# Performance work log

Measured on AMD Instinct MI355X. Metric: run time of the kernel, lower is better.

The kernel has to match this reference:

```python
import jax, jax.numpy as jnp
import numpy as np

# FlowNetC correlation config (kernel_size=1 -> pointwise patch; pad == max_displacement)
PAD = 20
MAX_DISP = 20
STRIDE2 = 2


def setup_inputs() -> dict:
    key = jax.random.key(0)
    k1, k2 = jax.random.split(key)
    B, C, H, W = 4, 256, 96, 96
    input1 = jax.random.normal(k1, (B, C, H, W), dtype=jnp.float32)
    input2 = jax.random.normal(k2, (B, C, H, W), dtype=jnp.float32)
    return {"input1": input1, "input2": input2}


def _correlation(x1, x2):
    # x1, x2: [B, C, H, W]. Output: [B, D*D, H, W] with D = 2*MAX_DISP//STRIDE2 + 1.
    B, C, H, W = x1.shape
    x2p = jnp.pad(x2, ((0, 0), (0, 0), (PAD, PAD), (PAD, PAD)))
    D = 2 * MAX_DISP // STRIDE2 + 1  # 21
    # start index into padded map = PAD + (disp) where disp = off - MAX_DISP;
    # since PAD == MAX_DISP, start index == off.
    offs = jnp.arange(D, dtype=jnp.int32) * STRIDE2
    dyv, dxv = jnp.meshgrid(offs, offs, indexing="ij")
    pairs = jnp.stack([dyv.ravel(), dxv.ravel()], axis=1)  # [D*D, 2]
    inv_c = jnp.float32(1.0 / C)  # CUDA kernel divides by kernel^2 * C (kernel=1)

    def body(_, p):
        dy, dx = p[0], p[1]
        sl = jax.lax.dynamic_slice(x2p, (0, 0, dy, dx), (B, C, H, W))
        return None, jnp.einsum("bchw,bchw->bhw", x1, sl) * inv_c

    _, corr = jax.lax.scan(body, None, pairs)  # [D*D, B, H, W]
    return corr.transpose(1, 0, 2, 3)  # [B, D*D, H, W]


def reference(input1, input2):
    return _correlation(input1, input2)
```

## Files before the change

kernel.cpp:

```cpp
#include <hip/hip_runtime.h>
#include <hip/hip_bf16.h>


typedef __bf16 bf16x8 __attribute__((ext_vector_type(8)));
typedef float f32x4 __attribute__((ext_vector_type(4)));

#define B_ 4
#define C_ 256
#define H_ 96
#define W_ 96
#define NOFF 21
#define ROWS 96
#define IMG_ELEMS (ROWS * C_)
#define X1T_ELEMS (B_ * H_ * IMG_ELEMS)

__device__ __forceinline__ unsigned short f32_to_bf16_rne(float f) {
    union { float f; unsigned u; } v; v.f = f;
    unsigned u = v.u;
    return (unsigned short)((u + 0x7fffu + ((u >> 16) & 1u)) >> 16);
}

__device__ __forceinline__ void gl2lds16(const void* g, void* l) {
    __builtin_amdgcn_global_load_lds(
        (const __attribute__((address_space(1))) void*)g,
        (__attribute__((address_space(3))) void*)l, 16, 0, 0);
}

__global__ __launch_bounds__(256) void prep_kernel(const float* __restrict__ x1,
                                                   const float* __restrict__ x2,
                                                   unsigned short* __restrict__ ws) {
    __shared__ float tile[96 * 65];
    int bid = blockIdx.x;
    int cblk  = bid & 3;
    int which = (bid >> 2) & 1;
    int bh    = bid >> 3;
    int h = bh % H_;
    int b = bh / H_;
    int c0 = cblk << 6;

    const float* src = (which ? x2 : x1) + ((size_t)(b * C_ + c0) * H_ + h) * W_;
    unsigned short* dst = ws + (size_t)which * X1T_ELEMS + (size_t)(b * H_ + h) * IMG_ELEMS;

    for (int idx = threadIdx.x; idx < 64 * 96; idx += 256) {
        int c = idx / 96, w = idx - c * 96;
        tile[w * 65 + c] = src[c * (H_ * W_) + w];
    }
    __syncthreads();

    for (int idx = threadIdx.x; idx < 96 * 8; idx += 256) {
        int row = idx >> 3, tp = idx & 7;
        int par = row / 48, i = row - par * 48;
        int w = 2 * i + par;
        int s = tp ^ (row & 7);
        const float* fsrc = &tile[w * 65 + (s << 3)];
        unsigned pk[4];
#pragma unroll
        for (int e = 0; e < 4; ++e) {
            unsigned lo = f32_to_bf16_rne(fsrc[2 * e]);
            unsigned hi = f32_to_bf16_rne(fsrc[2 * e + 1]);
            pk[e] = lo | (hi << 16);
        }
        int ccp = (((c0 >> 3) ^ (row & 24)) + tp);
        *(uint4*)((char*)(dst + (size_t)row * C_) + (ccp << 4)) =
            make_uint4(pk[0], pk[1], pk[2], pk[3]);
    }
}

__global__ __launch_bounds__(384, 2) void corr_kernel(const unsigned short* __restrict__ ws,
                                                      float* __restrict__ out) {
    __shared__ unsigned short Bs[3][IMG_ELEMS];
    __shared__ float sl[2][NOFF][97];
    static_assert(sizeof(Bs) + sizeof(sl) <= 163840, "LDS budget");

    int bid = blockIdx.x;
    int xcd = bid & 7, sidx = bid >> 3;
    int b  = xcd >> 1;
    int p  = ((xcd & 1) ? 24 : 0) + (sidx >> 2);
    int og = sidx & 3;
    int g = p >> 1, par_h = p & 1;
    int hA = 4 * g + par_h, hB = hA + 2;
    int olo = (og * NOFF) >> 2;
    int ohi = ((og + 1) * NOFF) >> 2;

    int tid = threadIdx.x;
    int wv = tid >> 6, lane = tid & 63;
    int par = wv & 1, mt = wv >> 1;
    int i0 = mt << 4;
    int n = lane & 15, quad = lane >> 4;

    int jcnt = 5 + (tid < 96 ? 1 : 0);
    int slotj[6], offj[6]; bool mj[6];
#pragma unroll
    for (int j = 0; j < 6; ++j) {
        int idx = tid + j * 384;
        int ox = idx / W_, w = idx - ox * W_;
        slotj[j] = ox * 97 + w;
        offj[j]  = ox * (H_ * W_) + w;
        int w2 = w + 2 * ox - 20;
        mj[j] = (w2 >= 0) & (w2 < W_);
    }

    int rowA = par * 48 + i0 + n;
    int keyA = rowA & 31;
    const unsigned short* AgA = ws + (size_t)(b * H_ + hA) * IMG_ELEMS + (size_t)rowA * C_;
    const unsigned short* AgB = ws + (size_t)(b * H_ + hB) * IMG_ELEMS + (size_t)rowA * C_;
    bf16x8 afA[8], afB[8];
#pragma unroll
    for (int ks = 0; ks < 8; ++ks) {
        int o = (((ks << 2) | quad) ^ keyA) << 3;
        afA[ks] = *(const bf16x8*)(AgA + o);
        afB[ks] = *(const bf16x8*)(AgB + o);
    }

    const unsigned short* Bimg = ws + (size_t)X1T_ELEMS + (size_t)(b * H_) * IMG_ELEMS;

    int rowB0 = par * 48 + n;
    int rowB1 = rowB0 + 16;
    int rowB2 = rowB0 + 32;
    int keyB0 = rowB0 & 31, keyB1 = rowB1 & 31, keyB2 = rowB2 & 31;

    int aLo = (hA <= 20) ? ((21 - hA) >> 1) : 0; if (aLo < olo) aLo = olo;
    int aHi = ((115 - hA) >> 1) + 1;             if (aHi > ohi) aHi = ohi;
    if (aHi < aLo) aHi = aLo;
    int bLo = (hB <= 20) ? ((21 - hB) >> 1) : 0; if (bLo < olo) bLo = olo;
    int bHi = ((115 - hB) >> 1) + 1;             if (bHi > ohi) bHi = ohi;
    if (bHi < bLo) bHi = bLo;

    int tlo, thi;
    bool ea = (aLo >= aHi), eb = (bLo >= bHi);
    if (ea && eb)      { tlo = 0; thi = 0; }
    else if (ea)       { tlo = bLo + 1; thi = bHi + 1; }
    else if (eb)       { tlo = aLo; thi = aHi; }
    else {
        tlo = (aLo < bLo + 1) ? aLo : bLo + 1;
        thi = (aHi > bHi + 1) ? aHi : bHi + 1;
    }
    int nv = thi - tlo;

    int wvoff  = wv * 8192;
    int gmaoff = wvoff + lane * 16;

    if (nv > 0) {
        const char* Bg = (const char*)(Bimg + (size_t)(hA + 2 * tlo - 20) * IMG_ELEMS);
#pragma unroll
        for (int c = 0; c < 8; ++c)
            gl2lds16(Bg + gmaoff + c * 1024, (char*)Bs[0] + wvoff + c * 1024);
    }
    if (nv > 1) {
        const char* Bg = (const char*)(Bimg + (size_t)(hA + 2 * (tlo + 1) - 20) * IMG_ELEMS);
#pragma unroll
        for (int c = 0; c < 8; ++c)
            gl2lds16(Bg + gmaoff + c * 1024, (char*)Bs[1] + wvoff + c * 1024);
    }

    for (int oy = olo; oy < ohi; ++oy) {
        if (oy < aLo || oy >= aHi) {
            int outb = ((b * 441 + oy * NOFF) * H_ + hA) * W_;
#pragma unroll
            for (int j = 0; j < 6; ++j) if (j < jcnt) out[outb + offj[j]] = 0.0f;
        }
        if (oy < bLo || oy >= bHi) {
            int outb = ((b * 441 + oy * NOFF) * H_ + hB) * W_;
#pragma unroll
            for (int j = 0; j < 6; ++j) if (j < jcnt) out[outb + offj[j]] = 0.0f;
        }
    }

    const float* slA = &sl[0][0][0];
    const float* slB = &sl[1][0][0];

    for (int k = 0; k < nv; ++k) {
        int t = tlo + k;
        int cur = k % 3;

        if (k + 2 < nv) {
            int nb = (k + 2) % 3;
            const char* Bg = (const char*)(Bimg + (size_t)(hA + 2 * (t + 2) - 20) * IMG_ELEMS);
#pragma unroll
            for (int c = 0; c < 8; ++c)
                gl2lds16(Bg + gmaoff + c * 1024, (char*)Bs[nb] + wvoff + c * 1024);
        }

        if (k == 0) {
            if (nv > 2)       asm volatile("s_waitcnt vmcnt(16)\ns_barrier" ::: "memory");
            else if (nv == 2) asm volatile("s_waitcnt vmcnt(8)\ns_barrier" ::: "memory");
            else              asm volatile("s_waitcnt vmcnt(0)\ns_barrier" ::: "memory");
        } else if (k + 2 < nv) {
            asm volatile("s_waitcnt vmcnt(21)\ns_barrier" ::: "memory");
        } else if (k + 1 < nv) {
            asm volatile("s_waitcnt vmcnt(13)\ns_barrier" ::: "memory");
        } else {
            asm volatile("s_waitcnt vmcnt(5)\ns_barrier" ::: "memory");
        }

        const char* Bsb = (const char*)Bs[cur];
        f32x4 aA0 = {0.f,0.f,0.f,0.f}, aA1 = {0.f,0.f,0.f,0.f}, aA2 = {0.f,0.f,0.f,0.f};
        f32x4 aB0 = {0.f,0.f,0.f,0.f}, aB1 = {0.f,0.f,0.f,0.f}, aB2 = {0.f,0.f,0.f,0.f};

        if (mt == 0) {
            bf16x8 f0[8], f1[8];
#pragma unroll
            for (int ks = 0; ks < 8; ++ks) {
                int ci = (ks << 2) | quad;
                f0[ks] = *(const bf16x8*)(Bsb + rowB0 * 512 + ((ci ^ keyB0) << 4));
                f1[ks] = *(const bf16x8*)(Bsb + rowB1 * 512 + ((ci ^ keyB1) << 4));
            }
#pragma unroll
            for (int ks = 0; ks < 8; ++ks) {
                aA0 = __builtin_amdgcn_mfma_f32_16x16x32_bf16(afA[ks], f0[ks], aA0, 0, 0, 0);
                aA1 = __builtin_amdgcn_mfma_f32_16x16x32_bf16(afA[ks], f1[ks], aA1, 0, 0, 0);
                aB0 = __builtin_amdgcn_mfma_f32_16x16x32_bf16(afB[ks], f0[ks], aB0, 0, 0, 0);
                aB1 = __builtin_amdgcn_mfma_f32_16x16x32_bf16(afB[ks], f1[ks], aB1, 0, 0, 0);
            }
        } else if (mt == 1) {
            bf16x8 f0[8], f1[8], f2[8];
#pragma unroll
            for (int ks = 0; ks < 8; ++ks) {
                int ci = (ks << 2) | quad;
                f0[ks] = *(const bf16x8*)(Bsb + rowB0 * 512 + ((ci ^ keyB0) << 4));
                f1[ks] = *(const bf16x8*)(Bsb + rowB1 * 512 + ((ci ^ keyB1) << 4));
                f2[ks] = *(const bf16x8*)(Bsb + rowB2 * 512 + ((ci ^ keyB2) << 4));
            }
#pragma unroll
            for (int ks = 0; ks < 8; ++ks) {
                aA0 = __builtin_amdgcn_mfma_f32_16x16x32_bf16(afA[ks], f0[ks], aA0, 0, 0, 0);
                aA1 = __builtin_amdgcn_mfma_f32_16x16x32_bf16(afA[ks], f1[ks], aA1, 0, 0, 0);
                aA2 = __builtin_amdgcn_mfma_f32_16x16x32_bf16(afA[ks], f2[ks], aA2, 0, 0, 0);
                aB0 = __builtin_amdgcn_mfma_f32_16x16x32_bf16(afB[ks], f0[ks], aB0, 0, 0, 0);
                aB1 = __builtin_amdgcn_mfma_f32_16x16x32_bf16(afB[ks], f1[ks], aB1, 0, 0, 0);
                aB2 = __builtin_amdgcn_mfma_f32_16x16x32_bf16(afB[ks], f2[ks], aB2, 0, 0, 0);
            }
        } else {
            bf16x8 f1[8], f2[8];
#pragma unroll
            for (int ks = 0; ks < 8; ++ks) {
                int ci = (ks << 2) | quad;
                f1[ks] = *(const bf16x8*)(Bsb + rowB1 * 512 + ((ci ^ keyB1) << 4));
                f2[ks] = *(const bf16x8*)(Bsb + rowB2 * 512 + ((ci ^ keyB2) << 4));
            }
#pragma unroll
            for (int ks = 0; ks < 8; ++ks) {
                aA1 = __builtin_amdgcn_mfma_f32_16x16x32_bf16(afA[ks], f1[ks], aA1, 0, 0, 0);
                aA2 = __builtin_amdgcn_mfma_f32_16x16x32_bf16(afA[ks], f2[ks], aA2, 0, 0, 0);
                aB1 = __builtin_amdgcn_mfma_f32_16x16x32_bf16(afB[ks], f1[ks], aB1, 0, 0, 0);
                aB2 = __builtin_amdgcn_mfma_f32_16x16x32_bf16(afB[ks], f2[ks], aB2, 0, 0, 0);
            }
        }

#pragma unroll
        for (int r = 0; r < 4; ++r) {
            int m = (quad << 2) + r;
            int w = 2 * (i0 + m) + par;
            int oxb = n - i0 - m - 6;
            if (mt != 2) { int ox = 16 + oxb; if (ox >= 0 && ox < NOFF) { sl[0][ox][w] = aA0[r]; sl[1][ox][w] = aB0[r]; } }
            {             int ox = 32 + oxb; if (ox >= 0 && ox < NOFF) { sl[0][ox][w] = aA1[r]; sl[1][ox][w] = aB1[r]; } }
            if (mt != 0) { int ox = 48 + oxb; if (ox >= 0 && ox < NOFF) { sl[0][ox][w] = aA2[r]; sl[1][ox][w] = aB2[r]; } }
        }

        asm volatile("s_waitcnt lgkmcnt(0)\ns_barrier" ::: "memory");

        bool okA = (t >= aLo) & (t < aHi);
        bool okB = (t - 1 >= bLo) & (t - 1 < bHi);
        int outbA = ((b * 441 + t * NOFF) * H_ + hA) * W_;
        int outbB = ((b * 441 + (t - 1) * NOFF) * H_ + hB) * W_;

        float vA[6], vB[6];
#pragma unroll
        for (int j = 0; j < 6; ++j) if (j < jcnt) {
            vA[j] = mj[j] ? slA[slotj[j]] * (1.0f / 256.0f) : 0.0f;
            vB[j] = mj[j] ? slB[slotj[j]] * (1.0f / 256.0f) : 0.0f;
        }
        if (okA) {
#pragma unroll
            for (int j = 0; j < 6; ++j) if (j < jcnt) out[outbA + offj[j]] = vA[j];
        }
        if (okB) {
#pragma unroll
            for (int j = 0; j < 6; ++j) if (j < jcnt) out[outbB + offj[j]] = vB[j];
        }
    }
}

__global__ __launch_bounds__(256) void corr_fallback(const float* __restrict__ x1,
                                                     const float* __restrict__ x2,
                                                     float* __restrict__ out) {
    int bid = blockIdx.x;
    int oy = bid % NOFF, h = (bid / NOFF) % H_, b = bid / (NOFF * H_);
    int dy = 2 * oy - 20, h2 = h + dy;
    int outbase = ((b * 441 + oy * NOFF) * H_ + h) * W_;
    for (int idx = threadIdx.x; idx < NOFF * W_; idx += 256) {
        int ox = idx / W_, w = idx % W_;
        float acc = 0.f;
        int w2 = w + 2 * ox - 20;
        if (h2 >= 0 && h2 < H_ && w2 >= 0 && w2 < W_) {
            const float* p1 = x1 + (size_t)b * C_ * H_ * W_ + h * W_ + w;
            const float* p2 = x2 + (size_t)b * C_ * H_ * W_ + h2 * W_ + w2;
            for (int c = 0; c < C_; ++c) acc += p1[c * (H_ * W_)] * p2[c * (H_ * W_)];
        }
        out[outbase + ox * (H_ * W_) + w] = acc * (1.0f / 256.0f);
    }
}

extern "C" void kernel_launch(void* const* d_in, const int* in_sizes, int n_in,
                              void* d_out, int out_size, void* d_ws, size_t ws_size,
                              hipStream_t stream) {
    const float* x1 = (const float*)d_in[0];
    const float* x2 = (const float*)d_in[1];
    float* out = (float*)d_out;

    size_t need = (size_t)2 * X1T_ELEMS * sizeof(unsigned short);
    if (ws_size >= need) {
        unsigned short* ws = (unsigned short*)d_ws;
        prep_kernel<<<B_ * H_ * 2 * 4, 256, 0, stream>>>(x1, x2, ws);
        corr_kernel<<<768, 384, 0, stream>>>(ws, out);
    } else {
        corr_fallback<<<B_ * H_ * NOFF, 256, 0, stream>>>(x1, x2, out);
    }
}
```

Baseline: 164.6 us.

## Single-buffer LDS tile to fit more blocks per CU, prefetch after barrier

```diff
diff --git a/kernel.cpp b/kernel.cpp
--- a/kernel.cpp
+++ b/kernel.cpp
@@ -66,11 +66,11 @@
     }
 }
 
-__global__ __launch_bounds__(384, 2) void corr_kernel(const unsigned short* __restrict__ ws,
+__global__ __launch_bounds__(384, 3) void corr_kernel(const unsigned short* __restrict__ ws,
                                                       float* __restrict__ out) {
-    __shared__ unsigned short Bs[3][IMG_ELEMS];
+    __shared__ unsigned short Bs[IMG_ELEMS];
     __shared__ float sl[2][NOFF][97];
-    static_assert(sizeof(Bs) + sizeof(sl) <= 163840, "LDS budget");
+    static_assert(sizeof(Bs) + sizeof(sl) <= 81920, "need 2 blocks/CU");
 
     int bid = blockIdx.x;
     int xcd = bid & 7, sidx = bid >> 3;
@@ -111,6 +111,8 @@
         afA[ks] = *(const bf16x8*)(AgA + o);
         afB[ks] = *(const bf16x8*)(AgB + o);
     }
+    asm volatile("" ::: "memory");
+    __builtin_amdgcn_s_waitcnt(0);
 
     const unsigned short* Bimg = ws + (size_t)X1T_ELEMS + (size_t)(b * H_) * IMG_ELEMS;
 
@@ -140,18 +142,15 @@
     int wvoff  = wv * 8192;
     int gmaoff = wvoff + lane * 16;
 
-    if (nv > 0) {
-        const char* Bg = (const char*)(Bimg + (size_t)(hA + 2 * tlo - 20) * IMG_ELEMS);
-#pragma unroll
-        for (int c = 0; c < 8; ++c)
-            gl2lds16(Bg + gmaoff + c * 1024, (char*)Bs[0] + wvoff + c * 1024);
-    }
-    if (nv > 1) {
-        const char* Bg = (const char*)(Bimg + (size_t)(hA + 2 * (tlo + 1) - 20) * IMG_ELEMS);
-#pragma unroll
-        for (int c = 0; c < 8; ++c)
-            gl2lds16(Bg + gmaoff + c * 1024, (char*)Bs[1] + wvoff + c * 1024);
-    }
+#define STAGE(tt) do {                                                                \
+    const char* Bg_ = (const char*)(Bimg + (size_t)(hA + 2 * (tt) - 20) * IMG_ELEMS); \
+    _Pragma("unroll")                                                                 \
+    for (int c = 0; c < 8; ++c)                                                       \
+        gl2lds16(Bg_ + gmaoff + c * 1024, (char*)Bs + wvoff + c * 1024);              \
+} while (0)
+
+    if (nv > 0) STAGE(tlo);
+    asm volatile("" ::: "memory");
 
     for (int oy = olo; oy < ohi; ++oy) {
         if (oy < aLo || oy >= aHi) {
@@ -171,32 +170,15 @@
 
     for (int k = 0; k < nv; ++k) {
         int t = tlo + k;
-        int cur = k % 3;
-
-        if (k + 2 < nv) {
-            int nb = (k + 2) % 3;
-            const char* Bg = (const char*)(Bimg + (size_t)(hA + 2 * (t + 2) - 20) * IMG_ELEMS);
-#pragma unroll
-            for (int c = 0; c < 8; ++c)
-                gl2lds16(Bg + gmaoff + c * 1024, (char*)Bs[nb] + wvoff + c * 1024);
-        }
-
-        if (k == 0) {
-            if (nv > 2)       asm volatile("s_waitcnt vmcnt(16)\ns_barrier" ::: "memory");
-            else if (nv == 2) asm volatile("s_waitcnt vmcnt(8)\ns_barrier" ::: "memory");
-            else              asm volatile("s_waitcnt vmcnt(0)\ns_barrier" ::: "memory");
-        } else if (k + 2 < nv) {
-            asm volatile("s_waitcnt vmcnt(21)\ns_barrier" ::: "memory");
-        } else if (k + 1 < nv) {
-            asm volatile("s_waitcnt vmcnt(13)\ns_barrier" ::: "memory");
-        } else {
-            asm volatile("s_waitcnt vmcnt(5)\ns_barrier" ::: "memory");
-        }
-
-        const char* Bsb = (const char*)Bs[cur];
+
+        if (k == 0) asm volatile("s_waitcnt vmcnt(0)\ns_barrier" ::: "memory");
+        else        asm volatile("s_waitcnt vmcnt(5)\ns_barrier" ::: "memory");
+
+        const char* Bsb = (const char*)Bs;
         f32x4 aA0 = {0.f,0.f,0.f,0.f}, aA1 = {0.f,0.f,0.f,0.f}, aA2 = {0.f,0.f,0.f,0.f};
         f32x4 aB0 = {0.f,0.f,0.f,0.f}, aB1 = {0.f,0.f,0.f,0.f}, aB2 = {0.f,0.f,0.f,0.f};
 
+        __builtin_amdgcn_s_setprio(1);
         if (mt == 0) {
             bf16x8 f0[8], f1[8];
 #pragma unroll
@@ -246,6 +228,7 @@
                 aB2 = __builtin_amdgcn_mfma_f32_16x16x32_bf16(afB[ks], f2[ks], aB2, 0, 0, 0);
             }
         }
+        __builtin_amdgcn_s_setprio(0);
 
 #pragma unroll
         for (int r = 0; r < 4; ++r) {
@@ -259,6 +242,9 @@
 
         asm volatile("s_waitcnt lgkmcnt(0)\ns_barrier" ::: "memory");
 
+        if (k + 1 < nv) STAGE(t + 1);
+        asm volatile("" ::: "memory");
+
         bool okA = (t >= aLo) & (t < aHi);
         bool okB = (t - 1 >= bLo) & (t - 1 < bHi);
         int outbA = ((b * 441 + t * NOFF) * H_ + hA) * W_;
@@ -279,6 +265,7 @@
             for (int j = 0; j < 6; ++j) if (j < jcnt) out[outbB + offj[j]] = vB[j];
         }
     }
+#undef STAGE
 }
 
 __global__ __launch_bounds__(256) void corr_fallback(const float* __restrict__ x1,
```

New measurement: 163.1 us. No clear change (-1.0%).
